# Kernel optimization log

Measured on AMD Instinct MI355X. Metric: run time of the kernel, lower is better.

Reference implementation:

```python
import jax, jax.numpy as jnp
import numpy as np

N, C, H, W = 2, 4, 112, 112
IGNORE = 0  # HD_IGNORE_CLASS_INDEX


def setup_inputs() -> dict:
    key = jax.random.key(0)
    k1, k2 = jax.random.split(key)
    predictions = jax.random.normal(k1, (N, C, H, W), dtype=jnp.float32)
    labels = jax.random.randint(k2, (N, C, H, W), 0, 2, dtype=jnp.int32)
    return {"predictions": predictions, "labels": labels}


def _pixel_dist_matrix(h, w):
    # Euclidean distance between all pairs of (row, col) pixel coordinates,
    # identical to cdist(argwhere(...), argwhere(...)) restricted by masks.
    rr, cc = jnp.meshgrid(jnp.arange(h, dtype=jnp.float32),
                          jnp.arange(w, dtype=jnp.float32), indexing="ij")
    r = rr.reshape(-1)
    c = cc.reshape(-1)
    return jnp.sqrt((r[:, None] - r[None, :]) ** 2 + (c[:, None] - c[None, :]) ** 2)  # (HW, HW)


def reference(predictions, labels):
    # F.softmax + argmax + one-hot -> per-class boolean prediction masks
    probs = jax.nn.softmax(predictions, axis=1)
    pred_cls = jnp.argmax(probs, axis=1)  # (N, H, W) int

    D = _pixel_dist_matrix(H, W)  # (HW, HW), data-independent

    fhd = jnp.zeros(C + 2, jnp.float32)
    rhd = jnp.zeros(C + 2, jnp.float32)
    mhd = jnp.zeros(C + 2, jnp.float32)

    for b in range(N):
        for j in range(C):
            if j == IGNORE:
                continue
            A = (pred_cls[b] == j).reshape(-1)        # predicted point set mask (HW,)
            Bm = (labels[b, j] == 1).reshape(-1)      # label point set mask (HW,)
            Af = A.astype(jnp.float32)
            Bf = Bm.astype(jnp.float32)
            # forward: mean over A-points of min distance to B-points
            rowmin = jnp.min(jnp.where(Bm[None, :], D, jnp.inf), axis=1)  # (HW,)
            fwd = jnp.sum(rowmin * Af) / jnp.sum(Af)
            # reverse: mean over B-points of min distance to A-points
            colmin = jnp.min(jnp.where(A[:, None], D, jnp.inf), axis=0)   # (HW,)
            rev = jnp.sum(colmin * Bf) / jnp.sum(Bf)
            fhd = fhd.at[j].add(fwd)
            rhd = rhd.at[j].add(rev)
            mhd = mhd.at[j].add(jnp.maximum(fwd, rev))

    def finalize(x):
        x = x.at[:C].divide(jnp.float32(N))
        x = x.at[C].set(jnp.mean(x[:C]))
        x = x.at[C + 1].set(jnp.mean(x[1:C]))
        return x

    return (finalize(mhd), finalize(fhd), finalize(rhd))
```

## Files before the change

### kernel.cpp

```cpp
#include <hip/hip_runtime.h>
#include <hip/hip_bf16.h>
#include <cstdint>
#include <climits>

#define HW 112
#define NPIX (HW*HW)
#define NB 2
#define NC 4
#define CHUNKS 28
#define HD_GRID (12*CHUNKS)


__global__ __launch_bounds__(128) void prep_kernel(
    const float* __restrict__ pred, const int* __restrict__ labels,
    unsigned long long* __restrict__ masks, unsigned short* __restrict__ gsqbuf)
{
  int blk = blockIdx.x;
  int b = blk / HW, r = blk % HW;
  int tid = threadIdx.x;
  int lane = tid & 63, wave = tid >> 6;
  int c = tid;

  int cls = 255;
  if (c < HW) {
    const float* p0 = pred + ((size_t)(b*NC)*HW + r)*HW + c;
    float best = p0[0]; cls = 0;
    #pragma unroll
    for (int ch = 1; ch < NC; ch++) {
      float v = p0[(size_t)ch*NPIX];
      if (v > best) { best = v; cls = ch; }
    }
  }

  __shared__ unsigned long long sm[6][2];
  #pragma unroll
  for (int m = 0; m < 3; m++) {
    bool p = (c < HW) && (cls == m + 1);
    unsigned long long bal = __ballot(p);
    if (lane == 0) sm[m][wave] = bal;
  }
  #pragma unroll
  for (int m = 0; m < 3; m++) {
    int lab = (c < HW) ? labels[((size_t)(b*NC + (m+1))*HW + r)*HW + c] : 0;
    bool p = (c < HW) && (lab == 1);
    unsigned long long bal = __ballot(p);
    if (lane == 0) sm[3 + m][wave] = bal;
  }
  __syncthreads();

  if (tid < 12) {
    int m = tid >> 1, w = tid & 1;
    masks[((size_t)(b*6 + m)*HW + r)*2 + w] = sm[m][w];
  }

  for (int item = tid; item < 6*HW; item += 128) {
    int m = item / HW, cc = item % HW;
    unsigned long long lo = sm[m][0], hi = sm[m][1];
    int left, right;
    if (cc < 64) {
      unsigned long long wl = lo & ((2ull << cc) - 1);
      left = wl ? 63 - __clzll(wl) : -1000;
      unsigned long long wr = lo & ~((1ull << cc) - 1);
      right = wr ? __ffsll(wr) - 1 : (hi ? 64 + __ffsll(hi) - 1 : 1000);
    } else {
      int cl = cc - 64;
      unsigned long long wl = hi & ((2ull << cl) - 1);
      left = wl ? 64 + 63 - __clzll(wl) : (lo ? 63 - __clzll(lo) : -1000);
      unsigned long long wr = hi & ~((1ull << cl) - 1);
      right = wr ? 64 + __ffsll(wr) - 1 : 1000;
    }
    int gv = min(min(cc - left, right - cc), 255);
    gsqbuf[(size_t)(b*6 + m)*NPIX + r*HW + cc] = (unsigned short)(gv*gv);
  }
}

__global__ __launch_bounds__(128) void hd_kernel(
    const unsigned long long* __restrict__ masks,
    const unsigned short* __restrict__ gsqbuf,
    float2* __restrict__ partial)
{
  int blk = blockIdx.x;
  int pd = blk / CHUNKS, chunk = blk % CHUNKS;
  int b = pd / 6, k = pd % 6;
  int src = b*6 + (k + 3) % 6;
  int tid = threadIdx.x, lane = tid & 63, wv = tid >> 6;
  int c = tid;
  int r0 = chunk * 4;

  float sum = 0.f, cf = 0.f;
  if (c < HW) {
    const unsigned short* g2p = gsqbuf + (size_t)src*NPIX + c;

    int w[8];
    #pragma unroll
    for (int t = 0; t < 8; t++) {
      int gr = r0 - 2 + t;
      w[t] = (gr >= 0 && gr < HW) ? (int)g2p[(size_t)gr*HW] : 0x7fff;
    }

    #pragma unroll
    for (int i = 0; i < 4; i++) {
      int r = r0 + i;
      int best = w[i + 2];
      best = min(best, 1 + min(w[i + 1], w[i + 3]));
      best = min(best, 4 + min(w[i],     w[i + 4]));
      if (best > 9) {
        for (int d = 3; d < HW; d++) {
          int dd = d*d;
          if (dd >= best) break;
          int ru = r - d, rd = r + d;
          if (ru >= 0)  best = min(best, dd + (int)g2p[(size_t)ru*HW]);
          if (rd < HW)  best = min(best, dd + (int)g2p[(size_t)rd*HW]);
        }
      }
      unsigned long long wm = masks[((size_t)pd*HW + r)*2 + (c >> 6)];
      if ((wm >> (c & 63)) & 1ull) { sum += sqrtf((float)best); cf += 1.f; }
    }
  }

  #pragma unroll
  for (int off = 32; off; off >>= 1) {
    sum += __shfl_down(sum, off, 64);
    cf  += __shfl_down(cf, off, 64);
  }
  __shared__ float red[4];
  if (lane == 0) { red[wv*2] = sum; red[wv*2 + 1] = cf; }
  __syncthreads();
  if (tid == 0) partial[blk] = make_float2(red[0] + red[2], red[1] + red[3]);
}

__global__ __launch_bounds__(768) void fin_kernel(
    const float2* __restrict__ partial, float* __restrict__ out)
{
  int tid = threadIdx.x;
  int w = tid >> 6, lane = tid & 63;
  __shared__ float sacc[24];

  float s = 0.f, cnt = 0.f;
  if (lane < CHUNKS) {
    float2 p = partial[w*CHUNKS + lane];
    s = p.x; cnt = p.y;
  }
  #pragma unroll
  for (int off = 32; off; off >>= 1) {
    s   += __shfl_down(s, off, 64);
    cnt += __shfl_down(cnt, off, 64);
  }
  if (lane == 0) { sacc[w] = s; sacc[12 + w] = cnt; }
  __syncthreads();

  if (tid == 0) {
    float mhd[6], fhd[6], rhd[6];
    for (int i = 0; i < 6; i++) { mhd[i] = 0.f; fhd[i] = 0.f; rhd[i] = 0.f; }
    for (int bb = 0; bb < 2; bb++)
      for (int j = 1; j < 4; j++) {
        int pf = bb*6 + (j - 1);
        int pr = bb*6 + 3 + (j - 1);
        float fwd = sacc[pf] / sacc[12 + pf];
        float rev = sacc[pr] / sacc[12 + pr];
        fhd[j] += fwd; rhd[j] += rev; mhd[j] += fmaxf(fwd, rev);
      }
    float* arrs[3] = { mhd, fhd, rhd };
    for (int a = 0; a < 3; a++) {
      float* x = arrs[a];
      for (int i = 0; i < 4; i++) x[i] *= 0.5f;
      x[4] = (x[0] + x[1] + x[2] + x[3]) * 0.25f;
      x[5] = (x[1] + x[2] + x[3]) * (1.f / 3.f);
      for (int i = 0; i < 6; i++) out[a*6 + i] = x[i];
    }
  }
}

extern "C" void kernel_launch(void* const* d_in, const int* in_sizes, int n_in,
                              void* d_out, int out_size, void* d_ws, size_t ws_size,
                              hipStream_t stream) {
  const float* pred = (const float*)d_in[0];
  const int* labels = (const int*)d_in[1];
  float* out = (float*)d_out;

  unsigned long long* masks = (unsigned long long*)d_ws;
  unsigned short* gsqbuf = (unsigned short*)((char*)d_ws + 21504);
  float2* partial = (float2*)((char*)d_ws + 21504 + (size_t)12*NPIX*sizeof(unsigned short));

  prep_kernel<<<NB*HW, 128, 0, stream>>>(pred, labels, masks, gsqbuf);
  hd_kernel<<<HD_GRID, 128, 0, stream>>>(masks, gsqbuf, partial);
  fin_kernel<<<1, 768, 0, stream>>>(partial, out);
}
```

Measured before the change: 14.92 us.

## Fuse final reduction into HD kernel via last-block atomic counter

Removes the separate finalize kernel: each of the now 24 blocks (1024 threads, 8 row-groups of 7 rows per half image) writes its partial sums, bumps a global counter, and the last block to finish computes the output metrics. The counter is reset inside prep_kernel. The vertical window is now a sliding register window per row group, so each row is loaded once instead of from a fixed 8-row tile. This saves one kernel launch, at the cost of fewer, larger blocks and atomic and fence traffic.

Result: slower. 16.98 us (+13.8%).

```diff
diff --git a/kernel.cpp b/kernel.cpp
--- a/kernel.cpp
+++ b/kernel.cpp
@@ -7,19 +7,22 @@
 #define NPIX (HW*HW)
 #define NB 2
 #define NC 4
-#define CHUNKS 28
-#define HD_GRID (12*CHUNKS)
+#define HALF_ROWS 56
+#define HD_BLKS 24
 
 
 __global__ __launch_bounds__(128) void prep_kernel(
     const float* __restrict__ pred, const int* __restrict__ labels,
-    unsigned long long* __restrict__ masks, unsigned short* __restrict__ gsqbuf)
+    unsigned long long* __restrict__ masks, unsigned short* __restrict__ gsqbuf,
+    unsigned* __restrict__ counter)
 {
   int blk = blockIdx.x;
   int b = blk / HW, r = blk % HW;
   int tid = threadIdx.x;
   int lane = tid & 63, wave = tid >> 6;
   int c = tid;
+
+  if (blk == 0 && tid == 0) *counter = 0;
 
   int cls = 255;
   if (c < HW) {
@@ -74,36 +77,36 @@
   }
 }
 
-__global__ __launch_bounds__(128) void hd_kernel(
+__device__ __forceinline__ int g2row(const unsigned short* __restrict__ g2p, int row) {
+  return (row >= 0 && row < HW) ? (int)g2p[(size_t)row*HW] : 0x7fff;
+}
+
+__global__ __launch_bounds__(1024) void hd_kernel(
     const unsigned long long* __restrict__ masks,
     const unsigned short* __restrict__ gsqbuf,
-    float2* __restrict__ partial)
+    float* __restrict__ S, float* __restrict__ Cc,
+    unsigned* __restrict__ counter, float* __restrict__ out)
 {
   int blk = blockIdx.x;
-  int pd = blk / CHUNKS, chunk = blk % CHUNKS;
+  int pd = blk >> 1, half = blk & 1;
   int b = pd / 6, k = pd % 6;
   int src = b*6 + (k + 3) % 6;
   int tid = threadIdx.x, lane = tid & 63, wv = tid >> 6;
-  int c = tid;
-  int r0 = chunk * 4;
+  int rg = tid / HW, c = tid % HW;
 
   float sum = 0.f, cf = 0.f;
-  if (c < HW) {
+  if (rg < 8) {
     const unsigned short* g2p = gsqbuf + (size_t)src*NPIX + c;
-
-    int w[8];
-    #pragma unroll
-    for (int t = 0; t < 8; t++) {
-      int gr = r0 - 2 + t;
-      w[t] = (gr >= 0 && gr < HW) ? (int)g2p[(size_t)gr*HW] : 0x7fff;
-    }
-
-    #pragma unroll
-    for (int i = 0; i < 4; i++) {
-      int r = r0 + i;
-      int best = w[i + 2];
-      best = min(best, 1 + min(w[i + 1], w[i + 3]));
-      best = min(best, 4 + min(w[i],     w[i + 4]));
+    int rbase = half*HALF_ROWS + rg*7;
+    int vm2 = g2row(g2p, rbase - 2), vm1 = g2row(g2p, rbase - 1);
+    int v0  = g2row(g2p, rbase),     vp1 = g2row(g2p, rbase + 1);
+    int vp2 = g2row(g2p, rbase + 2);
+    #pragma unroll 7
+    for (int i = 0; i < 7; i++) {
+      int r = rbase + i;
+      int best = v0;
+      best = min(best, 1 + min(vm1, vp1));
+      best = min(best, 4 + min(vm2, vp2));
       if (best > 9) {
         for (int d = 3; d < HW; d++) {
           int dd = d*d;
@@ -115,6 +118,7 @@
       }
       unsigned long long wm = masks[((size_t)pd*HW + r)*2 + (c >> 6)];
       if ((wm >> (c & 63)) & 1ull) { sum += sqrtf((float)best); cf += 1.f; }
+      vm2 = vm1; vm1 = v0; v0 = vp1; vp1 = vp2; vp2 = g2row(g2p, r + 3);
     }
   }
 
@@ -123,50 +127,53 @@
     sum += __shfl_down(sum, off, 64);
     cf  += __shfl_down(cf, off, 64);
   }
-  __shared__ float red[4];
+  __shared__ float red[32];
+  __shared__ int isLast;
   if (lane == 0) { red[wv*2] = sum; red[wv*2 + 1] = cf; }
   __syncthreads();
-  if (tid == 0) partial[blk] = make_float2(red[0] + red[2], red[1] + red[3]);
-}
-
-__global__ __launch_bounds__(768) void fin_kernel(
-    const float2* __restrict__ partial, float* __restrict__ out)
-{
-  int tid = threadIdx.x;
-  int w = tid >> 6, lane = tid & 63;
-  __shared__ float sacc[24];
-
-  float s = 0.f, cnt = 0.f;
-  if (lane < CHUNKS) {
-    float2 p = partial[w*CHUNKS + lane];
-    s = p.x; cnt = p.y;
+  if (tid == 0) {
+    float Sv = 0.f, Cv = 0.f;
+    #pragma unroll
+    for (int w = 0; w < 16; w++) { Sv += red[w*2]; Cv += red[w*2 + 1]; }
+    atomicExch(&S[blk], Sv);
+    atomicExch(&Cc[blk], Cv);
+    __threadfence();
+    unsigned old = atomicAdd(counter, 1u);
+    isLast = (old == HD_BLKS - 1) ? 1 : 0;
   }
-  #pragma unroll
-  for (int off = 32; off; off >>= 1) {
-    s   += __shfl_down(s, off, 64);
-    cnt += __shfl_down(cnt, off, 64);
-  }
-  if (lane == 0) { sacc[w] = s; sacc[12 + w] = cnt; }
   __syncthreads();
 
-  if (tid == 0) {
-    float mhd[6], fhd[6], rhd[6];
-    for (int i = 0; i < 6; i++) { mhd[i] = 0.f; fhd[i] = 0.f; rhd[i] = 0.f; }
-    for (int bb = 0; bb < 2; bb++)
-      for (int j = 1; j < 4; j++) {
-        int pf = bb*6 + (j - 1);
-        int pr = bb*6 + 3 + (j - 1);
-        float fwd = sacc[pf] / sacc[12 + pf];
-        float rev = sacc[pr] / sacc[12 + pr];
-        fhd[j] += fwd; rhd[j] += rev; mhd[j] += fmaxf(fwd, rev);
+  if (isLast) {
+    __shared__ float fs[HD_BLKS], fc[HD_BLKS], sacc[24];
+    if (tid < HD_BLKS) {
+      fs[tid] = atomicAdd(&S[tid], 0.0f);
+      fc[tid] = atomicAdd(&Cc[tid], 0.0f);
+    }
+    __syncthreads();
+    if (tid < 12) {
+      sacc[tid]      = fs[tid*2] + fs[tid*2 + 1];
+      sacc[12 + tid] = fc[tid*2] + fc[tid*2 + 1];
+    }
+    __syncthreads();
+    if (tid == 0) {
+      float mhd[6], fhd[6], rhd[6];
+      for (int i = 0; i < 6; i++) { mhd[i] = 0.f; fhd[i] = 0.f; rhd[i] = 0.f; }
+      for (int bb = 0; bb < 2; bb++)
+        for (int j = 1; j < 4; j++) {
+          int pf = bb*6 + (j - 1);
+          int pr = bb*6 + 3 + (j - 1);
+          float fwd = sacc[pf] / sacc[12 + pf];
+          float rev = sacc[pr] / sacc[12 + pr];
+          fhd[j] += fwd; rhd[j] += rev; mhd[j] += fmaxf(fwd, rev);
+        }
+      float* arrs[3] = { mhd, fhd, rhd };
+      for (int a = 0; a < 3; a++) {
+        float* x = arrs[a];
+        for (int i = 0; i < 4; i++) x[i] *= 0.5f;
+        x[4] = (x[0] + x[1] + x[2] + x[3]) * 0.25f;
+        x[5] = (x[1] + x[2] + x[3]) * (1.f / 3.f);
+        for (int i = 0; i < 6; i++) out[a*6 + i] = x[i];
       }
-    float* arrs[3] = { mhd, fhd, rhd };
-    for (int a = 0; a < 3; a++) {
-      float* x = arrs[a];
-      for (int i = 0; i < 4; i++) x[i] *= 0.5f;
-      x[4] = (x[0] + x[1] + x[2] + x[3]) * 0.25f;
-      x[5] = (x[1] + x[2] + x[3]) * (1.f / 3.f);
-      for (int i = 0; i < 6; i++) out[a*6 + i] = x[i];
     }
   }
 }
@@ -180,9 +187,10 @@
 
   unsigned long long* masks = (unsigned long long*)d_ws;
   unsigned short* gsqbuf = (unsigned short*)((char*)d_ws + 21504);
-  float2* partial = (float2*)((char*)d_ws + 21504 + (size_t)12*NPIX*sizeof(unsigned short));
+  float* S  = (float*)((char*)d_ws + 322560);
+  float* Cc = (float*)((char*)d_ws + 322656);
+  unsigned* counter = (unsigned*)((char*)d_ws + 322752);
 
-  prep_kernel<<<NB*HW, 128, 0, stream>>>(pred, labels, masks, gsqbuf);
-  hd_kernel<<<HD_GRID, 128, 0, stream>>>(masks, gsqbuf, partial);
-  fin_kernel<<<1, 768, 0, stream>>>(partial, out);
+  prep_kernel<<<NB*HW, 128, 0, stream>>>(pred, labels, masks, gsqbuf, counter);
+  hd_kernel<<<HD_BLKS, 1024, 0, stream>>>(masks, gsqbuf, S, Cc, counter, out);
 }
```
